# Kernel tuning notes

Measured on AMD Instinct MI355X. Metric: run time of the kernel, lower is better.

Reference implementation:

```python
import jax, jax.numpy as jnp
import numpy as np


def setup_inputs() -> dict:
    key = jax.random.key(0)
    k1, k2 = jax.random.split(key)
    B, D, H, W = 32, 64, 32, 32
    K = 1024
    z_e = jax.random.normal(k1, (B, D, H, W), dtype=jnp.float32)
    # original init: uniform(-1/K, 1/K); use same scale
    emb = jax.random.uniform(k2, (K, D), dtype=jnp.float32, minval=-1.0 / K, maxval=1.0 / K)
    return {"z_e": z_e, "emb": emb}


COMMITMENT_COST = 0.25


def reference(z_e, emb):
    # z_e: [B, D, H, W], emb: [K, D]
    B, D, H, W = z_e.shape
    K = emb.shape[0]
    z = jnp.transpose(z_e, (0, 2, 3, 1))           # [B, H, W, D]
    flat = z.reshape(-1, D)                        # [N, D]
    N = flat.shape[0]

    dist = (
        jnp.sum(flat * flat, axis=1, keepdims=True)
        + jnp.sum(emb * emb, axis=1)
        - 2.0 * flat @ emb.T
    )
    idx = jnp.argmin(dist, axis=1)                 # [N]
    encodings = jax.nn.one_hot(idx, K, dtype=flat.dtype)  # [N, K]
    z_q = (encodings @ emb).reshape(z.shape)       # [B, H, W, D]

    e_latent_loss = jnp.mean((jax.lax.stop_gradient(z_q) - z) ** 2)
    q_latent_loss = jnp.mean((z_q - jax.lax.stop_gradient(z)) ** 2)
    loss = q_latent_loss + COMMITMENT_COST * e_latent_loss

    # straight-through estimator
    z_st = z + jax.lax.stop_gradient(z_q - z)

    avg_probs = jnp.sum(encodings, axis=0) / jnp.float32(N)
    perplexity = jnp.exp(-jnp.sum(avg_probs * jnp.log(avg_probs + 1e-10)))

    return (jnp.transpose(z_st, (0, 3, 1, 2)), loss, perplexity, encodings)
```

## Files before the change

kernel.cpp:

```cpp
#include <hip/hip_runtime.h>
#include <stdint.h>
#include <math.h>

constexpr int Nn  = 32768;
constexpr int Kk  = 1024;

constexpr int OUT0_N   = 32 * 64 * 1024;
constexpr int OUT_LOSS = OUT0_N;
constexpr int OUT_PERP = OUT0_N + 1;
constexpr int OUT_ENC  = OUT0_N + 2;

constexpr size_t WS_CNT = 0;
constexpr size_t WS_LP  = 4096;
constexpr size_t WS_KEY = 69632;

__device__ __forceinline__ float norm64v(const float4* __restrict__ p) {
#pragma clang fp contract(off)
    float tt[64];
#pragma unroll
    for (int q = 0; q < 16; ++q) {
        float4 v = p[q];
        tt[4 * q + 0] = v.x * v.x;
        tt[4 * q + 1] = v.y * v.y;
        tt[4 * q + 2] = v.z * v.z;
        tt[4 * q + 3] = v.w * v.w;
    }
    float r[8];
#pragma unroll
    for (int j = 0; j < 8; ++j) r[j] = tt[j];
#pragma unroll
    for (int i = 8; i < 64; i += 8)
#pragma unroll
        for (int j = 0; j < 8; ++j) r[j] += tt[i + j];
    return ((r[0] + r[1]) + (r[2] + r[3])) + ((r[4] + r[5]) + (r[6] + r[7]));
}

__device__ __forceinline__ uint32_t fsort(float f) {
    uint32_t b = __float_as_uint(f);
    return (b & 0x80000000u) ? ~b : (b | 0x80000000u);
}

__global__ __launch_bounds__(256, 2)
void dist_kernel(const float* __restrict__ z_e, const float* __restrict__ emb,
                 unsigned long long* __restrict__ minkey) {
    __shared__ float xs[128 * 68];
    __shared__ float es[128 * 68];
    __shared__ float An_s[128];
    __shared__ float Bn_s[128];
    const int tid = threadIdx.x;
    const int rg = blockIdx.x >> 3, cg = blockIdx.x & 7;
    const int n0 = rg * 128;
    const int b = n0 >> 10, hw0 = n0 & 1023;
    const float* zb = z_e + (size_t)b * 65536 + hw0;

    {
        int hwi = tid & 127;
        int d4g = tid >> 7;
#pragma unroll
        for (int it = 0; it < 8; ++it) {
            int dbase = (d4g + it * 2) * 4;
            float4 v;
            v.x = zb[(size_t)(dbase + 0) * 1024 + hwi];
            v.y = zb[(size_t)(dbase + 1) * 1024 + hwi];
            v.z = zb[(size_t)(dbase + 2) * 1024 + hwi];
            v.w = zb[(size_t)(dbase + 3) * 1024 + hwi];
            *(float4*)&xs[hwi * 68 + dbase] = v;
        }
    }
    {
        const float4* ep = (const float4*)(emb + (size_t)cg * 128 * 64);
#pragma unroll
        for (int it = 0; it < 8; ++it) {
            int j = tid + it * 256;
            float4 v = ep[j];
            int c = j >> 4, d4 = j & 15;
            *(float4*)&es[c * 68 + d4 * 4] = v;
        }
    }
    __syncthreads();

    if (tid < 128) {
        An_s[tid] = norm64v((const float4*)&xs[tid * 68]);
    } else {
        int c = tid - 128;
        Bn_s[c] = norm64v((const float4*)&es[c * 68]);
    }
    __syncthreads();

    const int tx = tid & 15, ty = tid >> 4;
    float acc[8][8];
#pragma unroll
    for (int i = 0; i < 8; ++i)
#pragma unroll
        for (int j = 0; j < 8; ++j) acc[i][j] = 0.0f;

#pragma unroll 1
    for (int d4 = 0; d4 < 16; ++d4) {
        float4 xv[8], ev[8];
#pragma unroll
        for (int i = 0; i < 8; ++i) xv[i] = *(const float4*)&xs[(ty + 16 * i) * 68 + d4 * 4];
#pragma unroll
        for (int j = 0; j < 8; ++j) ev[j] = *(const float4*)&es[(tx + 16 * j) * 68 + d4 * 4];
#pragma unroll
        for (int i = 0; i < 8; ++i)
#pragma unroll
            for (int j = 0; j < 8; ++j) {
                float a = acc[i][j];
                a = __builtin_fmaf(xv[i].x, ev[j].x, a);
                a = __builtin_fmaf(xv[i].y, ev[j].y, a);
                a = __builtin_fmaf(xv[i].z, ev[j].z, a);
                a = __builtin_fmaf(xv[i].w, ev[j].w, a);
                acc[i][j] = a;
            }
    }

    float Ar[8], Bc[8];
#pragma unroll
    for (int i = 0; i < 8; ++i) Ar[i] = An_s[ty + 16 * i];
#pragma unroll
    for (int j = 0; j < 8; ++j) Bc[j] = Bn_s[tx + 16 * j];

#pragma unroll
    for (int i = 0; i < 8; ++i) {
        unsigned long long best = ~0ULL;
#pragma unroll
        for (int j = 0; j < 8; ++j) {
            float s = Ar[i] + Bc[j];
            float dist = s - 2.0f * acc[i][j];
            unsigned long long key = ((unsigned long long)fsort(dist) << 32)
                                   | (unsigned)(cg * 128 + tx + 16 * j);
            best = (key < best) ? key : best;
        }
#pragma unroll
        for (int m = 1; m < 16; m <<= 1) {
            unsigned long long o = __shfl_xor(best, m, 64);
            best = (o < best) ? o : best;
        }
        if (tx == 0) atomicMin(&minkey[n0 + ty + 16 * i], best);
    }
}

__global__ void finish_kernel(const float* __restrict__ z_e,
                              const float* __restrict__ emb,
                              const unsigned long long* __restrict__ minkey,
                              uint32_t* __restrict__ counts,
                              double* __restrict__ lp,
                              float* __restrict__ out) {
    __shared__ uint32_t scode[4];
    __shared__ double lred[4];
    const int t = threadIdx.x;
    const int r4 = blockIdx.x * 4;
    if (t < 4) {
        uint32_t code = (uint32_t)minkey[r4 + t];
        scode[t] = code;
        atomicAdd(&counts[code], 1u);
    }
    __syncthreads();

    {
        const int b = r4 >> 10, hw = (r4 & 1023) + (t & 3);
        const int d = t >> 2;
        const size_t off = (size_t)b * 65536 + (size_t)d * 1024 + hw;
        float z  = z_e[off];
        float zq = emb[(size_t)scode[t & 3] * 64 + d];
        float tt = zq - z;
        out[off] = z + tt;
        double ls = (double)tt * (double)tt;
#pragma unroll
        for (int m = 32; m >= 1; m >>= 1) ls += __shfl_down(ls, m, 64);
        if ((t & 63) == 0) lred[t >> 6] = ls;
    }
    __syncthreads();
    if (t == 0) lp[blockIdx.x] = lred[0] + lred[1] + lred[2] + lred[3];

    float* enc = out + OUT_ENC;
#pragma unroll
    for (int i = 0; i < 4; ++i) {
        uint32_t code = scode[i];
        uint32_t c0 = (uint32_t)(t * 4);
        float4 v;
        v.x = (code == c0 + 0u) ? 1.0f : 0.0f;
        v.y = (code == c0 + 1u) ? 1.0f : 0.0f;
        v.z = (code == c0 + 2u) ? 1.0f : 0.0f;
        v.w = (code == c0 + 3u) ? 1.0f : 0.0f;
        ((float4*)enc)[(size_t)(r4 + i) * 256 + t] = v;
    }
}

__global__ void scalar_kernel(const uint32_t* __restrict__ counts,
                              const double* __restrict__ lp,
                              float* __restrict__ out) {
    __shared__ double redl[4], redh[4];
    const int t = threadIdx.x;
    double ls = 0.0;
    for (int i = t; i < 8192; i += 256) ls += lp[i];
    double h = 0.0;
    for (int i = t; i < Kk; i += 256) {
        double p = (double)counts[i] * (1.0 / 32768.0);
        h += p * log(p + 1e-10);
    }
#pragma unroll
    for (int m = 32; m >= 1; m >>= 1) { ls += __shfl_down(ls, m, 64); h += __shfl_down(h, m, 64); }
    if ((t & 63) == 0) { redl[t >> 6] = ls; redh[t >> 6] = h; }
    __syncthreads();
    if (t == 0) {
        double L = redl[0] + redl[1] + redl[2] + redl[3];
        double H = redh[0] + redh[1] + redh[2] + redh[3];
        out[OUT_PERP] = (float)exp(-H);
        float m32 = (float)(L * (1.0 / 2097152.0));
        out[OUT_LOSS] = m32 + 0.25f * m32;
    }
}

extern "C" void kernel_launch(void* const* d_in, const int* in_sizes, int n_in,
                              void* d_out, int out_size, void* d_ws, size_t ws_size,
                              hipStream_t stream) {
    const float* z_e = (const float*)d_in[0];
    const float* emb = (const float*)d_in[1];
    float* out = (float*)d_out;
    char* ws = (char*)d_ws;

    uint32_t* counts = (uint32_t*)(ws + WS_CNT);
    double*   lp     = (double*)(ws + WS_LP);
    unsigned long long* minkey = (unsigned long long*)(ws + WS_KEY);

    hipMemsetAsync(ws + WS_CNT, 0, 4096, stream);
    hipMemsetAsync(ws + WS_KEY, 0xFF, (size_t)Nn * 8, stream);

    dist_kernel<<<2048, 256, 0, stream>>>(z_e, emb, minkey);
    finish_kernel<<<8192, 256, 0, stream>>>(z_e, emb, minkey, counts, lp, out);
    scalar_kernel<<<1, 256, 0, stream>>>(counts, lp, out);
}
```

Baseline: 236.3 us.

## Restructure distance kernel to read codebook via wave-uniform loads and move histogram

The distance GEMM no longer stages the codebook in shared memory. Each wave takes 32 codes and reads the embedding values with wave-uniform (scalar) global loads, and each lane computes 2 rows from a transposed x tile. A cross-wave shared-memory min reduction replaces the shuffle reduction, and occupancy is raised to 4 blocks per CU. The code histogram moves from global atomics in finish_kernel to a shared-memory histogram in the single-block scalar kernel, which drops a memset. The risks are lower FMA-to-load reuse (2x8 per thread instead of 8x8) and a serial single-block pass over 32K keys.

```diff
diff --git a/kernel.cpp b/kernel.cpp
--- a/kernel.cpp
+++ b/kernel.cpp
@@ -10,9 +10,8 @@
 constexpr int OUT_PERP = OUT0_N + 1;
 constexpr int OUT_ENC  = OUT0_N + 2;
 
-constexpr size_t WS_CNT = 0;
-constexpr size_t WS_LP  = 4096;
-constexpr size_t WS_KEY = 69632;
+constexpr size_t WS_LP  = 0;
+constexpr size_t WS_KEY = 65536;
 
 __device__ __forceinline__ float norm64v(const float4* __restrict__ p) {
 #pragma clang fp contract(off)
@@ -35,18 +34,39 @@
     return ((r[0] + r[1]) + (r[2] + r[3])) + ((r[4] + r[5]) + (r[6] + r[7]));
 }
 
+__device__ __forceinline__ float norm64s(const float4* __restrict__ p) {
+#pragma clang fp contract(off)
+    float tt[64];
+#pragma unroll
+    for (int q = 0; q < 16; ++q) {
+        float4 v = p[(size_t)q * 128];
+        tt[4 * q + 0] = v.x * v.x;
+        tt[4 * q + 1] = v.y * v.y;
+        tt[4 * q + 2] = v.z * v.z;
+        tt[4 * q + 3] = v.w * v.w;
+    }
+    float r[8];
+#pragma unroll
+    for (int j = 0; j < 8; ++j) r[j] = tt[j];
+#pragma unroll
+    for (int i = 8; i < 64; i += 8)
+#pragma unroll
+        for (int j = 0; j < 8; ++j) r[j] += tt[i + j];
+    return ((r[0] + r[1]) + (r[2] + r[3])) + ((r[4] + r[5]) + (r[6] + r[7]));
+}
+
 __device__ __forceinline__ uint32_t fsort(float f) {
     uint32_t b = __float_as_uint(f);
     return (b & 0x80000000u) ? ~b : (b | 0x80000000u);
 }
 
-__global__ __launch_bounds__(256, 2)
+__global__ __launch_bounds__(256, 4)
 void dist_kernel(const float* __restrict__ z_e, const float* __restrict__ emb,
                  unsigned long long* __restrict__ minkey) {
-    __shared__ float xs[128 * 68];
-    __shared__ float es[128 * 68];
+    __shared__ float4 xs[16 * 128];
     __shared__ float An_s[128];
     __shared__ float Bn_s[128];
+    __shared__ unsigned long long best4[4 * 128];
     const int tid = threadIdx.x;
     const int rg = blockIdx.x >> 3, cg = blockIdx.x & 7;
     const int n0 = rg * 128;
@@ -58,103 +78,103 @@
         int d4g = tid >> 7;
 #pragma unroll
         for (int it = 0; it < 8; ++it) {
-            int dbase = (d4g + it * 2) * 4;
+            int d4 = d4g + it * 2;
+            int dbase = d4 * 4;
             float4 v;
             v.x = zb[(size_t)(dbase + 0) * 1024 + hwi];
             v.y = zb[(size_t)(dbase + 1) * 1024 + hwi];
             v.z = zb[(size_t)(dbase + 2) * 1024 + hwi];
             v.w = zb[(size_t)(dbase + 3) * 1024 + hwi];
-            *(float4*)&xs[hwi * 68 + dbase] = v;
-        }
-    }
-    {
-        const float4* ep = (const float4*)(emb + (size_t)cg * 128 * 64);
-#pragma unroll
-        for (int it = 0; it < 8; ++it) {
-            int j = tid + it * 256;
-            float4 v = ep[j];
-            int c = j >> 4, d4 = j & 15;
-            *(float4*)&es[c * 68 + d4 * 4] = v;
+            xs[d4 * 128 + hwi] = v;
         }
     }
     __syncthreads();
 
     if (tid < 128) {
-        An_s[tid] = norm64v((const float4*)&xs[tid * 68]);
+        An_s[tid] = norm64s(&xs[tid]);
     } else {
         int c = tid - 128;
-        Bn_s[c] = norm64v((const float4*)&es[c * 68]);
-    }
-    __syncthreads();
-
-    const int tx = tid & 15, ty = tid >> 4;
-    float acc[8][8];
-#pragma unroll
-    for (int i = 0; i < 8; ++i)
-#pragma unroll
-        for (int j = 0; j < 8; ++j) acc[i][j] = 0.0f;
+        Bn_s[c] = norm64v((const float4*)(emb + (size_t)(cg * 128 + c) * 64));
+    }
+    __syncthreads();
+
+    const int w = __builtin_amdgcn_readfirstlane(tid >> 6);
+    const int l = tid & 63;
+    const int cb = cg * 128 + w * 32;
+    const float An0 = An_s[l];
+    const float An1 = An_s[l + 64];
+    const float* eb = emb + (size_t)cb * 64;
+
+    unsigned long long b0 = ~0ULL, b1 = ~0ULL;
 
 #pragma unroll 1
-    for (int d4 = 0; d4 < 16; ++d4) {
-        float4 xv[8], ev[8];
-#pragma unroll
-        for (int i = 0; i < 8; ++i) xv[i] = *(const float4*)&xs[(ty + 16 * i) * 68 + d4 * 4];
-#pragma unroll
-        for (int j = 0; j < 8; ++j) ev[j] = *(const float4*)&es[(tx + 16 * j) * 68 + d4 * 4];
-#pragma unroll
-        for (int i = 0; i < 8; ++i)
-#pragma unroll
-            for (int j = 0; j < 8; ++j) {
-                float a = acc[i][j];
-                a = __builtin_fmaf(xv[i].x, ev[j].x, a);
-                a = __builtin_fmaf(xv[i].y, ev[j].y, a);
-                a = __builtin_fmaf(xv[i].z, ev[j].z, a);
-                a = __builtin_fmaf(xv[i].w, ev[j].w, a);
-                acc[i][j] = a;
+    for (int g = 0; g < 4; ++g) {
+        const float* eg = eb + g * 8 * 64;
+        float a0[8], a1[8];
+#pragma unroll
+        for (int c = 0; c < 8; ++c) { a0[c] = 0.0f; a1[c] = 0.0f; }
+
+#pragma unroll 2
+        for (int d4 = 0; d4 < 16; ++d4) {
+            float4 x0 = xs[d4 * 128 + l];
+            float4 x1 = xs[d4 * 128 + l + 64];
+#pragma unroll
+            for (int c = 0; c < 8; ++c) {
+                const float* ec = eg + c * 64 + d4 * 4;
+                float e0 = ec[0], e1 = ec[1], e2 = ec[2], e3 = ec[3];
+                float t0 = a0[c];
+                t0 = __builtin_fmaf(x0.x, e0, t0);
+                t0 = __builtin_fmaf(x0.y, e1, t0);
+                t0 = __builtin_fmaf(x0.z, e2, t0);
+                t0 = __builtin_fmaf(x0.w, e3, t0);
+                a0[c] = t0;
+                float t1 = a1[c];
+                t1 = __builtin_fmaf(x1.x, e0, t1);
+                t1 = __builtin_fmaf(x1.y, e1, t1);
+                t1 = __builtin_fmaf(x1.z, e2, t1);
+                t1 = __builtin_fmaf(x1.w, e3, t1);
+                a1[c] = t1;
             }
-    }
-
-    float Ar[8], Bc[8];
-#pragma unroll
-    for (int i = 0; i < 8; ++i) Ar[i] = An_s[ty + 16 * i];
-#pragma unroll
-    for (int j = 0; j < 8; ++j) Bc[j] = Bn_s[tx + 16 * j];
-
-#pragma unroll
-    for (int i = 0; i < 8; ++i) {
-        unsigned long long best = ~0ULL;
-#pragma unroll
-        for (int j = 0; j < 8; ++j) {
-            float s = Ar[i] + Bc[j];
-            float dist = s - 2.0f * acc[i][j];
-            unsigned long long key = ((unsigned long long)fsort(dist) << 32)
-                                   | (unsigned)(cg * 128 + tx + 16 * j);
-            best = (key < best) ? key : best;
-        }
-#pragma unroll
-        for (int m = 1; m < 16; m <<= 1) {
-            unsigned long long o = __shfl_xor(best, m, 64);
-            best = (o < best) ? o : best;
-        }
-        if (tx == 0) atomicMin(&minkey[n0 + ty + 16 * i], best);
+        }
+#pragma unroll
+        for (int c = 0; c < 8; ++c) {
+            float Bc = Bn_s[w * 32 + g * 8 + c];
+            unsigned code = (unsigned)(cb + g * 8 + c);
+            float s0 = An0 + Bc;
+            float d0 = s0 - 2.0f * a0[c];
+            unsigned long long k0 = ((unsigned long long)fsort(d0) << 32) | code;
+            b0 = (k0 < b0) ? k0 : b0;
+            float s1 = An1 + Bc;
+            float d1 = s1 - 2.0f * a1[c];
+            unsigned long long k1 = ((unsigned long long)fsort(d1) << 32) | code;
+            b1 = (k1 < b1) ? k1 : b1;
+        }
+    }
+
+    best4[w * 128 + l]      = b0;
+    best4[w * 128 + l + 64] = b1;
+    __syncthreads();
+    if (tid < 128) {
+        unsigned long long m = best4[tid];
+#pragma unroll
+        for (int ww = 1; ww < 4; ++ww) {
+            unsigned long long o = best4[ww * 128 + tid];
+            m = (o < m) ? o : m;
+        }
+        atomicMin(&minkey[n0 + tid], m);
     }
 }
 
 __global__ void finish_kernel(const float* __restrict__ z_e,
                               const float* __restrict__ emb,
                               const unsigned long long* __restrict__ minkey,
-                              uint32_t* __restrict__ counts,
                               double* __restrict__ lp,
                               float* __restrict__ out) {
     __shared__ uint32_t scode[4];
     __shared__ double lred[4];
     const int t = threadIdx.x;
     const int r4 = blockIdx.x * 4;
-    if (t < 4) {
-        uint32_t code = (uint32_t)minkey[r4 + t];
-        scode[t] = code;
-        atomicAdd(&counts[code], 1u);
-    }
+    if (t < 4) scode[t] = (uint32_t)minkey[r4 + t];
     __syncthreads();
 
     {
@@ -187,16 +207,21 @@
     }
 }
 
-__global__ void scalar_kernel(const uint32_t* __restrict__ counts,
+__global__ void scalar_kernel(const unsigned long long* __restrict__ minkey,
                               const double* __restrict__ lp,
                               float* __restrict__ out) {
+    __shared__ uint32_t hist[Kk];
     __shared__ double redl[4], redh[4];
     const int t = threadIdx.x;
+    for (int i = t; i < Kk; i += 256) hist[i] = 0;
+    __syncthreads();
+    for (int i = t; i < Nn; i += 256) atomicAdd(&hist[(uint32_t)minkey[i] & 1023u], 1u);
+    __syncthreads();
     double ls = 0.0;
     for (int i = t; i < 8192; i += 256) ls += lp[i];
     double h = 0.0;
     for (int i = t; i < Kk; i += 256) {
-        double p = (double)counts[i] * (1.0 / 32768.0);
+        double p = (double)hist[i] * (1.0 / 32768.0);
         h += p * log(p + 1e-10);
     }
 #pragma unroll
@@ -220,14 +245,12 @@
     float* out = (float*)d_out;
     char* ws = (char*)d_ws;
 
-    uint32_t* counts = (uint32_t*)(ws + WS_CNT);
-    double*   lp     = (double*)(ws + WS_LP);
+    double* lp = (double*)(ws + WS_LP);
     unsigned long long* minkey = (unsigned long long*)(ws + WS_KEY);
 
-    hipMemsetAsync(ws + WS_CNT, 0, 4096, stream);
     hipMemsetAsync(ws + WS_KEY, 0xFF, (size_t)Nn * 8, stream);
 
     dist_kernel<<<2048, 256, 0, stream>>>(z_e, emb, minkey);
-    finish_kernel<<<8192, 256, 0, stream>>>(z_e, emb, minkey, counts, lp, out);
-    scalar_kernel<<<1, 256, 0, stream>>>(counts, lp, out);
-}
+    finish_kernel<<<8192, 256, 0, stream>>>(z_e, emb, minkey, lp, out);
+    scalar_kernel<<<1, 256, 0, stream>>>(minkey, lp, out);
+}
```

New measurement: 337.2 us. 42.7% more time.
